# Kernel optimization log

Measured on AMD Instinct MI355X. Metric: run time of the kernel, lower is better.

The kernel has to match this reference:

```python
import jax, jax.numpy as jnp
import numpy as np

B, T, C = 2, 2048, 1024
H = 16
HD = C // H  # head_size = 64


def setup_inputs() -> dict:
    key = jax.random.key(0)
    k1, k2, k3 = jax.random.split(key, 3)
    x = jax.random.normal(k1, (B, T, C), dtype=jnp.float32)
    W_qkv = jax.random.normal(k2, (C, 3 * C), dtype=jnp.float32) * (1.0 / np.sqrt(C))
    b_qkv = jnp.zeros((3 * C,), dtype=jnp.float32)
    W_proj = jax.random.normal(k3, (C, C), dtype=jnp.float32) * (1.0 / np.sqrt(C))
    b_proj = jnp.zeros((C,), dtype=jnp.float32)
    return {"x": x, "W_qkv": W_qkv, "b_qkv": b_qkv, "W_proj": W_proj, "b_proj": b_proj}


def reference(x, W_qkv, b_qkv, W_proj, b_proj):
    Bc, Tc, Cc = x.shape
    qkv = x @ W_qkv + b_qkv                      # [B,T,3C]
    # Faithful to torch: view(B,T,H,3*HD) then chunk(3,-1) -> per-head interleaved split
    qkv = qkv.reshape(Bc, Tc, H, 3 * HD)
    q = qkv[..., 0 * HD:1 * HD]                  # [B,T,H,HD]
    k = qkv[..., 1 * HD:2 * HD]
    v = qkv[..., 2 * HD:3 * HD]
    # scores: [B,H,T,T]
    att = jnp.einsum('bqhd,bkhd->bhqk', q, k) / np.sqrt(HD)
    causal = jnp.tril(jnp.ones((Tc, Tc), dtype=bool))
    att = jnp.where(causal[None, None, :, :], att, -jnp.inf)
    att = jax.nn.softmax(att, axis=-1)
    out = jnp.einsum('bhqk,bkhd->bqhd', att, v).reshape(Bc, Tc, Cc)
    return out @ W_proj + b_proj
```

## Files before the change

### kernel.cpp

```cpp
#include <hip/hip_runtime.h>
#include <hip/hip_bf16.h>
#include <stdint.h>
#include <math.h>

#define T_SEQ 2048
#define NHEAD 16
#define CDIM 1024
#define QKV2_LD 2048

typedef __attribute__((ext_vector_type(8))) short short8;
typedef __attribute__((ext_vector_type(4))) short short4v;
typedef __attribute__((ext_vector_type(4))) float floatx4;

static __device__ __forceinline__ short bf16b(float f) {
    __hip_bfloat16 h = __float2bfloat16(f);
    return __builtin_bit_cast(short, h);
}

__device__ __forceinline__ void transpose_body(
    const float* __restrict__ in, __hip_bfloat16* __restrict__ out,
    int R, int C, int bx, int by, int tid)
{
    __shared__ short tile[64][65];
    const int r0 = by << 6;
    const int c0 = bx << 6;
    #pragma unroll
    for (int t = 0; t < 4; ++t) {
        int ch = t * 256 + tid;
        int rr = ch >> 4, cc = (ch & 15) << 2;
        float4 v = *(const float4*)(in + (size_t)(r0 + rr) * C + c0 + cc);
        tile[rr][cc + 0] = bf16b(v.x);
        tile[rr][cc + 1] = bf16b(v.y);
        tile[rr][cc + 2] = bf16b(v.z);
        tile[rr][cc + 3] = bf16b(v.w);
    }
    __syncthreads();
    #pragma unroll
    for (int t = 0; t < 2; ++t) {
        int ch = t * 256 + tid;
        int cc = ch >> 3, rr8 = (ch & 7) << 3;
        short8 v;
        #pragma unroll
        for (int j = 0; j < 8; ++j) v[j] = tile[rr8 + j][cc];
        *(short8*)(out + (size_t)(c0 + cc) * R + r0 + rr8) = v;
    }
}

__global__ __launch_bounds__(256) void prep_kernel(
    const float* __restrict__ x,     __hip_bfloat16* __restrict__ xb,
    const float* __restrict__ Wqkv,  __hip_bfloat16* __restrict__ WqkvT,
    const float* __restrict__ Wproj, __hip_bfloat16* __restrict__ WprojT)
{
    const int bid = blockIdx.x;
    const int tid = threadIdx.x;
    if (bid < 2048) {
        int i = (bid * 256 + tid) * 8;
        float4 a = *(const float4*)(x + i);
        float4 b = *(const float4*)(x + i + 4);
        short8 o;
        o[0] = bf16b(a.x); o[1] = bf16b(a.y); o[2] = bf16b(a.z); o[3] = bf16b(a.w);
        o[4] = bf16b(b.x); o[5] = bf16b(b.y); o[6] = bf16b(b.z); o[7] = bf16b(b.w);
        *(short8*)(xb + i) = o;
    } else if (bid < 2816) {
        int r = bid - 2048;
        transpose_body(Wqkv, WqkvT, 1024, 3072, r % 48, r / 48, tid);
    } else {
        int r = bid - 2816;
        transpose_body(Wproj, WprojT, 1024, 1024, r & 15, r >> 4, tid);
    }
}

template <int MI, int NI, int MINW, bool QKV, typename OutT>
__global__ __launch_bounds__(256, MINW) void gemm_bias_kernel(
    const __hip_bfloat16* __restrict__ A,
    const __hip_bfloat16* __restrict__ Bt,
    const float* __restrict__ bias,
    OutT* __restrict__ C,
    __hip_bfloat16* __restrict__ vT,
    int M, int N, int K)
{
    __shared__ short As[MI * 32 * 64];
    __shared__ short Bs[NI * 32 * 64];
    const int tid  = threadIdx.x;
    const int lane = tid & 63;
    const int w    = tid >> 6;
    const int quad = lane >> 4;
    const int c16  = lane & 15;
    const int m0 = blockIdx.x * (MI * 32);
    const int n0 = blockIdx.y * (NI * 32);
    const int wm = (w >> 1) * (MI * 16);
    const int wn = (w & 1) * (NI * 16);

    floatx4 acc[MI][NI] = {};

    for (int kt = 0; kt < K; kt += 64) {
        __syncthreads();
        #pragma unroll
        for (int r = 0; r < MI; ++r) {
            int ch = r * 256 + tid;
            int row = ch >> 3, k8 = (ch & 7) << 3;
            const __hip_bfloat16* ga = A + (size_t)(m0 + row) * K + kt + k8;
            __builtin_amdgcn_global_load_lds(
                (const __attribute__((address_space(1))) void*)ga,
                (__attribute__((address_space(3))) void*)&As[ch * 8], 16, 0, 0);
        }
        #pragma unroll
        for (int r = 0; r < NI; ++r) {
            int ch = r * 256 + tid;
            int row = ch >> 3, k8 = (ch & 7) << 3;
            const __hip_bfloat16* gb = Bt + (size_t)(n0 + row) * K + kt + k8;
            __builtin_amdgcn_global_load_lds(
                (const __attribute__((address_space(1))) void*)gb,
                (__attribute__((address_space(3))) void*)&Bs[ch * 8], 16, 0, 0);
        }
        __syncthreads();
        #pragma unroll
        for (int ko = 0; ko < 64; ko += 32) {
            short8 af[MI], bfr[NI];
            #pragma unroll
            for (int mi = 0; mi < MI; ++mi)
                af[mi] = *(const short8*)&As[(wm + mi * 16 + c16) * 64 + ko + quad * 8];
            #pragma unroll
            for (int ni = 0; ni < NI; ++ni)
                bfr[ni] = *(const short8*)&Bs[(wn + ni * 16 + c16) * 64 + ko + quad * 8];
            #pragma unroll
            for (int mi = 0; mi < MI; ++mi)
                #pragma unroll
                for (int ni = 0; ni < NI; ++ni)
                    acc[mi][ni] = __builtin_amdgcn_mfma_f32_16x16x32_bf16(
                        af[mi], bfr[ni], acc[mi][ni], 0, 0, 0);
        }
    }

    if constexpr (QKV) {
        const int colblk = (n0 + wn) >> 6;
        const int head = colblk / 3;
        const int kind = colblk % 3;
        const int b    = m0 >> 11;
        __syncthreads();
        if (kind == 2) {
            short* tp = (w < 2) ? &As[w * 4096] : &Bs[(w - 2) * 4096];
            #pragma unroll
            for (int mi = 0; mi < MI; ++mi)
                #pragma unroll
                for (int ni = 0; ni < NI; ++ni) {
                    int hd = ni * 16 + c16;
                    float bv = bias[n0 + wn + hd];
                    short4v pk;
                    #pragma unroll
                    for (int r2 = 0; r2 < 4; ++r2) pk[r2] = bf16b(acc[mi][ni][r2] + bv);
                    int tc = mi * 4 + quad;
                    *(short4v*)&tp[hd * 64 + ((tc ^ ((hd & 7) << 1)) << 2)] = pk;
                }
            const size_t vb2 = ((size_t)(b * 16 + head)) * 64 * T_SEQ;
            const int t0 = (m0 + wm) & 2047;
            #pragma unroll
            for (int it = 0; it < 8; ++it) {
                int hd = it * 8 + (lane >> 3);
                int tc2 = (lane & 7) << 1;
                short8 vv = *(const short8*)&tp[hd * 64 + ((tc2 ^ ((hd & 7) << 1)) << 2)];
                *(short8*)(vT + vb2 + (size_t)hd * T_SEQ + t0 + ((lane & 7) << 3)) = vv;
            }
        } else {
            const int cbase = head * 128 + kind * 64;
            #pragma unroll
            for (int mi = 0; mi < MI; ++mi)
                #pragma unroll
                for (int ni = 0; ni < NI; ++ni) {
                    float bv = bias[n0 + wn + ni * 16 + c16];
                    int col = cbase + ni * 16 + c16;
                    #pragma unroll
                    for (int r2 = 0; r2 < 4; ++r2) {
                        int row = m0 + wm + mi * 16 + quad * 4 + r2;
                        C[(size_t)row * QKV2_LD + col] = __float2bfloat16(acc[mi][ni][r2] + bv);
                    }
                }
        }
    } else {
        #pragma unroll
        for (int mi = 0; mi < MI; ++mi)
            #pragma unroll
            for (int ni = 0; ni < NI; ++ni) {
                int col = n0 + wn + ni * 16 + c16;
                float bv = bias[col];
                #pragma unroll
                for (int r2 = 0; r2 < 4; ++r2) {
                    int row = m0 + wm + mi * 16 + quad * 4 + r2;
                    float v = acc[mi][ni][r2] + bv;
                    if constexpr (__is_same(OutT, float)) {
                        C[(size_t)row * N + col] = v;
                    } else {
                        C[(size_t)row * N + col] = __float2bfloat16(v);
                    }
                }
            }
    }
}

__global__ __launch_bounds__(256, 2) void attn_kernel(
    const __hip_bfloat16* __restrict__ qkv,
    const __hip_bfloat16* __restrict__ vT,
    __hip_bfloat16* __restrict__ attn_out)
{
    __shared__ short Ks[2][64 * 64];
    __shared__ short Vs[2][64 * 64];
    __shared__ short Pl[4][16 * 64];

    const int hb = blockIdx.x;
    const int p  = blockIdx.y;
    const int h  = hb & 15;
    const int b  = hb >> 4;
    const int tid  = threadIdx.x;
    const int lane = tid & 63;
    const int w    = tid >> 6;
    const int quad = lane >> 4;
    const int c16  = lane & 15;

    const size_t rowbase = (size_t)b * T_SEQ;
    const size_t vbase   = (size_t)hb * 64 * T_SEQ;
    const int qtA = p, qtB = 31 - p;
    const int q0A = qtA << 6, q0B = qtB << 6;
    const int wrow = w << 4;
    const int hoff = h * 128;
    const int key  = c16 & 7;

    short8 qfA[2], qfB[2];
    #pragma unroll
    for (int ko = 0; ko < 2; ++ko) {
        qfA[ko] = *(const short8*)(qkv +
            (rowbase + q0A + wrow + c16) * QKV2_LD + hoff + ko * 32 + quad * 8);
        qfB[ko] = *(const short8*)(qkv +
            (rowbase + q0B + wrow + c16) * QKV2_LD + hoff + ko * 32 + quad * 8);
    }

    floatx4 OA[4] = {}, OB[4] = {};
    float lpA = 0.f, lpB = 0.f;
    const float sc = 0.125f * 1.4426950408889634f;
    const int nkt = qtB + 1;

    auto stage = [&](int kt, int bsel) {
        const int k0s = kt << 6;
        #pragma unroll
        for (int r = 0; r < 2; ++r) {
            int ch = r * 256 + tid;
            int krow = ch >> 3;
            int hc = (ch & 7) ^ (krow & 7);
            const __hip_bfloat16* g = qkv + (rowbase + k0s + krow) * QKV2_LD + hoff + 64 + hc * 8;
            __builtin_amdgcn_global_load_lds(
                (const __attribute__((address_space(1))) void*)g,
                (__attribute__((address_space(3))) void*)&Ks[bsel][ch * 8], 16, 0, 0);
        }
        #pragma unroll
        for (int r = 0; r < 2; ++r) {
            int ch = r * 256 + tid;
            int hd = ch >> 3;
            int kc = (ch & 7) ^ (hd & 7);
            const __hip_bfloat16* g = vT + vbase + (size_t)hd * T_SEQ + k0s + kc * 8;
            __builtin_amdgcn_global_load_lds(
                (const __attribute__((address_space(1))) void*)g,
                (__attribute__((address_space(3))) void*)&Vs[bsel][ch * 8], 16, 0, 0);
        }
    };

    stage(0, 0);
    int buf = 0;

    for (int kt = 0; kt < nkt; ++kt) {
        __syncthreads();
        if (kt + 1 < nkt) stage(kt + 1, buf ^ 1);

        short8 kf[2][4], vb[2][4];
        #pragma unroll
        for (int ko = 0; ko < 2; ++ko)
            #pragma unroll
            for (int ni = 0; ni < 4; ++ni) {
                int sl = ((4 * ko + quad) ^ key) << 3;
                kf[ko][ni] = *(const short8*)&Ks[buf][(ni * 16 + c16) * 64 + sl];
                vb[ko][ni] = *(const short8*)&Vs[buf][(ni * 16 + c16) * 64 + sl];
            }

        auto process = [&](const short8 (&qf)[2], floatx4 (&O)[4], float& lp, bool diag) {
            short* Pw = &Pl[w][0];
            floatx4 S[4] = {};
            #pragma unroll
            for (int ko = 0; ko < 2; ++ko)
                #pragma unroll
                for (int ni = 0; ni < 4; ++ni)
                    S[ni] = __builtin_amdgcn_mfma_f32_16x16x32_bf16(
                        kf[ko][ni], qf[ko], S[ni], 0, 0, 0);
            if (diag) {
                #pragma unroll
                for (int ni = 0; ni < 4; ++ni)
                    #pragma unroll
                    for (int r = 0; r < 4; ++r) {
                        bool msk = (ni * 16 + quad * 4 + r) > (wrow + c16);
                        float pe = msk ? 0.f : exp2f(S[ni][r] * sc);
                        S[ni][r] = pe;
                        lp += pe;
                    }
            } else {
                #pragma unroll
                for (int ni = 0; ni < 4; ++ni)
                    #pragma unroll
                    for (int r = 0; r < 4; ++r) {
                        float pe = exp2f(S[ni][r] * sc);
                        S[ni][r] = pe;
                        lp += pe;
                    }
            }
            #pragma unroll
            for (int ni = 0; ni < 4; ++ni) {
                short4v pk;
                #pragma unroll
                for (int r = 0; r < 4; ++r) pk[r] = bf16b(S[ni][r]);
                int pair = ni * 2 + (quad >> 1);
                int off = c16 * 64 + ((((pair ^ key) << 1) + (quad & 1)) << 2);
                *(short4v*)&Pw[off] = pk;
            }
            #pragma unroll
            for (int ko = 0; ko < 2; ++ko) {
                int off = c16 * 64 + (((ko * 4 + quad) ^ key) << 3);
                short8 pa = *(const short8*)&Pw[off];
                #pragma unroll
                for (int ni = 0; ni < 4; ++ni)
                    O[ni] = __builtin_amdgcn_mfma_f32_16x16x32_bf16(
                        vb[ko][ni], pa, O[ni], 0, 0, 0);
            }
        };

        process(qfB, OB, lpB, kt == qtB);
        if (kt <= qtA) process(qfA, OA, lpA, kt == qtA);
        buf ^= 1;
    }

    auto finish = [&](floatx4 (&O)[4], float lp, int q0) {
        float l = lp;
        l += __shfl_xor(l, 16);
        l += __shfl_xor(l, 32);
        float inv = 1.0f / l;
        size_t row = rowbase + q0 + wrow + c16;
        #pragma unroll
        for (int ni = 0; ni < 4; ++ni) {
            short4v o;
            #pragma unroll
            for (int r = 0; r < 4; ++r) o[r] = bf16b(O[ni][r] * inv);
            *(short4v*)(attn_out + row * CDIM + h * 64 + ni * 16 + quad * 4) = o;
        }
    };
    finish(OA, lpA, q0A);
    finish(OB, lpB, q0B);
}

extern "C" void kernel_launch(void* const* d_in, const int* in_sizes, int n_in,
                              void* d_out, int out_size, void* d_ws, size_t ws_size,
                              hipStream_t stream) {
    const float* x     = (const float*)d_in[0];
    const float* Wqkv  = (const float*)d_in[1];
    const float* bqkv  = (const float*)d_in[2];
    const float* Wproj = (const float*)d_in[3];
    const float* bproj = (const float*)d_in[4];
    float* out = (float*)d_out;

    __hip_bfloat16* xb     = (__hip_bfloat16*)d_ws;
    __hip_bfloat16* WqkvT  = xb     + (size_t)4096 * 1024;
    __hip_bfloat16* WprojT = WqkvT  + (size_t)3072 * 1024;
    __hip_bfloat16* qkv2   = WprojT + (size_t)1024 * 1024;
    __hip_bfloat16* vT     = qkv2   + (size_t)4096 * 2048;
    __hip_bfloat16* attn   = vT     + (size_t)32 * 64 * 2048;

    prep_kernel<<<3072, 256, 0, stream>>>(x, xb, Wqkv, WqkvT, Wproj, WprojT);
    gemm_bias_kernel<4, 4, 2, true, __hip_bfloat16>
        <<<dim3(4096 / 128, 3072 / 128), 256, 0, stream>>>(
        xb, WqkvT, bqkv, qkv2, vT, 4096, 3072, 1024);
    attn_kernel<<<dim3(32, 16), 256, 0, stream>>>(qkv2, vT, attn);
    gemm_bias_kernel<2, 2, 4, false, float>
        <<<dim3(4096 / 64, 1024 / 64), 256, 0, stream>>>(
        attn, WprojT, bproj, out, nullptr, 4096, 1024, 1024);
}
```

Measured before the change: 178.0 us.

## Split paired causal query tiles into one block per tile with heavier-first ordering

The attention kernel previously paired query tile p with tile 31-p in a single block, so every block did equal causal work and shared each K/V stage between two query tiles. Now each block handles one query tile, the grid doubles to 32x32, and blockIdx.y is reversed so the longest tiles are scheduled first. Launch bounds rise to 4 blocks per CU, which lowers register pressure since only one accumulator set is live. The trade-off is that each K/V tile is loaded from global memory about twice as often, in exchange for more parallelism and occupancy.

```diff
diff --git a/kernel.cpp b/kernel.cpp
--- a/kernel.cpp
+++ b/kernel.cpp
@@ -197,7 +197,7 @@
     }
 }
 
-__global__ __launch_bounds__(256, 2) void attn_kernel(
+__global__ __launch_bounds__(256, 4) void attn_kernel(
     const __hip_bfloat16* __restrict__ qkv,
     const __hip_bfloat16* __restrict__ vT,
     __hip_bfloat16* __restrict__ attn_out)
@@ -207,7 +207,7 @@
     __shared__ short Pl[4][16 * 64];
 
     const int hb = blockIdx.x;
-    const int p  = blockIdx.y;
+    const int qt = 31 - blockIdx.y;
     const int h  = hb & 15;
     const int b  = hb >> 4;
     const int tid  = threadIdx.x;
@@ -218,25 +218,21 @@
 
     const size_t rowbase = (size_t)b * T_SEQ;
     const size_t vbase   = (size_t)hb * 64 * T_SEQ;
-    const int qtA = p, qtB = 31 - p;
-    const int q0A = qtA << 6, q0B = qtB << 6;
+    const int q0   = qt << 6;
     const int wrow = w << 4;
     const int hoff = h * 128;
     const int key  = c16 & 7;
 
-    short8 qfA[2], qfB[2];
+    short8 qf[2];
     #pragma unroll
-    for (int ko = 0; ko < 2; ++ko) {
-        qfA[ko] = *(const short8*)(qkv +
-            (rowbase + q0A + wrow + c16) * QKV2_LD + hoff + ko * 32 + quad * 8);
-        qfB[ko] = *(const short8*)(qkv +
-            (rowbase + q0B + wrow + c16) * QKV2_LD + hoff + ko * 32 + quad * 8);
-    }
-
-    floatx4 OA[4] = {}, OB[4] = {};
-    float lpA = 0.f, lpB = 0.f;
+    for (int ko = 0; ko < 2; ++ko)
+        qf[ko] = *(const short8*)(qkv +
+            (rowbase + q0 + wrow + c16) * QKV2_LD + hoff + ko * 32 + quad * 8);
+
+    floatx4 O[4] = {};
+    float lp = 0.f;
     const float sc = 0.125f * 1.4426950408889634f;
-    const int nkt = qtB + 1;
+    const int nkt = qt + 1;
 
     auto stage = [&](int kt, int bsel) {
         const int k0s = kt << 6;
@@ -279,76 +275,70 @@
                 vb[ko][ni] = *(const short8*)&Vs[buf][(ni * 16 + c16) * 64 + sl];
             }
 
-        auto process = [&](const short8 (&qf)[2], floatx4 (&O)[4], float& lp, bool diag) {
-            short* Pw = &Pl[w][0];
-            floatx4 S[4] = {};
-            #pragma unroll
-            for (int ko = 0; ko < 2; ++ko)
-                #pragma unroll
-                for (int ni = 0; ni < 4; ++ni)
-                    S[ni] = __builtin_amdgcn_mfma_f32_16x16x32_bf16(
-                        kf[ko][ni], qf[ko], S[ni], 0, 0, 0);
-            if (diag) {
-                #pragma unroll
-                for (int ni = 0; ni < 4; ++ni)
-                    #pragma unroll
-                    for (int r = 0; r < 4; ++r) {
-                        bool msk = (ni * 16 + quad * 4 + r) > (wrow + c16);
-                        float pe = msk ? 0.f : exp2f(S[ni][r] * sc);
-                        S[ni][r] = pe;
-                        lp += pe;
-                    }
-            } else {
-                #pragma unroll
-                for (int ni = 0; ni < 4; ++ni)
-                    #pragma unroll
-                    for (int r = 0; r < 4; ++r) {
-                        float pe = exp2f(S[ni][r] * sc);
-                        S[ni][r] = pe;
-                        lp += pe;
-                    }
-            }
-            #pragma unroll
-            for (int ni = 0; ni < 4; ++ni) {
-                short4v pk;
-                #pragma unroll
-                for (int r = 0; r < 4; ++r) pk[r] = bf16b(S[ni][r]);
-                int pair = ni * 2 + (quad >> 1);
-                int off = c16 * 64 + ((((pair ^ key) << 1) + (quad & 1)) << 2);
-                *(short4v*)&Pw[off] = pk;
-            }
-            #pragma unroll
-            for (int ko = 0; ko < 2; ++ko) {
-                int off = c16 * 64 + (((ko * 4 + quad) ^ key) << 3);
-                short8 pa = *(const short8*)&Pw[off];
-                #pragma unroll
-                for (int ni = 0; ni < 4; ++ni)
-                    O[ni] = __builtin_amdgcn_mfma_f32_16x16x32_bf16(
-                        vb[ko][ni], pa, O[ni], 0, 0, 0);
-            }
-        };
-
-        process(qfB, OB, lpB, kt == qtB);
-        if (kt <= qtA) process(qfA, OA, lpA, kt == qtA);
+        short* Pw = &Pl[w][0];
+        floatx4 S[4] = {};
+        #pragma unroll
+        for (int ko = 0; ko < 2; ++ko)
+            #pragma unroll
+            for (int ni = 0; ni < 4; ++ni)
+                S[ni] = __builtin_amdgcn_mfma_f32_16x16x32_bf16(
+                    kf[ko][ni], qf[ko], S[ni], 0, 0, 0);
+
+        if (kt == qt) {
+            #pragma unroll
+            for (int ni = 0; ni < 4; ++ni)
+                #pragma unroll
+                for (int r = 0; r < 4; ++r) {
+                    bool msk = (ni * 16 + quad * 4 + r) > (wrow + c16);
+                    float pe = msk ? 0.f : exp2f(S[ni][r] * sc);
+                    S[ni][r] = pe;
+                    lp += pe;
+                }
+        } else {
+            #pragma unroll
+            for (int ni = 0; ni < 4; ++ni)
+                #pragma unroll
+                for (int r = 0; r < 4; ++r) {
+                    float pe = exp2f(S[ni][r] * sc);
+                    S[ni][r] = pe;
+                    lp += pe;
+                }
+        }
+
+        #pragma unroll
+        for (int ni = 0; ni < 4; ++ni) {
+            short4v pk;
+            #pragma unroll
+            for (int r = 0; r < 4; ++r) pk[r] = bf16b(S[ni][r]);
+            int pair = ni * 2 + (quad >> 1);
+            int off = c16 * 64 + ((((pair ^ key) << 1) + (quad & 1)) << 2);
+            *(short4v*)&Pw[off] = pk;
+        }
+
+        #pragma unroll
+        for (int ko = 0; ko < 2; ++ko) {
+            int off = c16 * 64 + (((ko * 4 + quad) ^ key) << 3);
+            short8 pa = *(const short8*)&Pw[off];
+            #pragma unroll
+            for (int ni = 0; ni < 4; ++ni)
+                O[ni] = __builtin_amdgcn_mfma_f32_16x16x32_bf16(
+                    vb[ko][ni], pa, O[ni], 0, 0, 0);
+        }
         buf ^= 1;
     }
 
-    auto finish = [&](floatx4 (&O)[4], float lp, int q0) {
-        float l = lp;
-        l += __shfl_xor(l, 16);
-        l += __shfl_xor(l, 32);
-        float inv = 1.0f / l;
-        size_t row = rowbase + q0 + wrow + c16;
-        #pragma unroll
-        for (int ni = 0; ni < 4; ++ni) {
-            short4v o;
-            #pragma unroll
-            for (int r = 0; r < 4; ++r) o[r] = bf16b(O[ni][r] * inv);
-            *(short4v*)(attn_out + row * CDIM + h * 64 + ni * 16 + quad * 4) = o;
-        }
-    };
-    finish(OA, lpA, q0A);
-    finish(OB, lpB, q0B);
+    float l = lp;
+    l += __shfl_xor(l, 16);
+    l += __shfl_xor(l, 32);
+    float inv = 1.0f / l;
+    size_t row = rowbase + q0 + wrow + c16;
+    #pragma unroll
+    for (int ni = 0; ni < 4; ++ni) {
+        short4v o;
+        #pragma unroll
+        for (int r = 0; r < 4; ++r) o[r] = bf16b(O[ni][r] * inv);
+        *(short4v*)(attn_out + row * CDIM + h * 64 + ni * 16 + quad * 4) = o;
+    }
 }
 
 extern "C" void kernel_launch(void* const* d_in, const int* in_sizes, int n_in,
@@ -372,7 +362,7 @@
     gemm_bias_kernel<4, 4, 2, true, __hip_bfloat16>
         <<<dim3(4096 / 128, 3072 / 128), 256, 0, stream>>>(
         xb, WqkvT, bqkv, qkv2, vT, 4096, 3072, 1024);
-    attn_kernel<<<dim3(32, 16), 256, 0, stream>>>(qkv2, vT, attn);
+    attn_kernel<<<dim3(32, 32), 256, 0, stream>>>(qkv2, vT, attn);
     gemm_bias_kernel<2, 2, 4, false, float>
         <<<dim3(4096 / 64, 1024 / 64), 256, 0, stream>>>(
         attn, WprojT, bproj, out, nullptr, 4096, 1024, 1024);
```

Measured after the change: 177.1 us. About the same (-0.5%).
